# Optimization experiments

Measured on AMD Instinct MI355X. Metric: run time of the kernel, lower is better.

Reference implementation:

```python
import jax, jax.numpy as jnp
import numpy as np

N = 50000          # neuron_count
NNZ = 1_600_000    # edges (avg degree 32)
B = 32             # batch
L = 3              # CONNECTOME_LAYER_NUMBER


def setup_inputs() -> dict:
    key = jax.random.key(0)
    k1, k2, k3, k4, k5 = jax.random.split(key, 5)
    x = jax.random.normal(k1, (B, N), dtype=jnp.float32)
    adj_vals = jax.random.uniform(k2, (NNZ,), dtype=jnp.float32)
    w_vals = jax.random.uniform(k3, (NNZ,), dtype=jnp.float32)
    bias = jnp.ones((N,), dtype=jnp.float32)
    row = jax.random.randint(k4, (NNZ,), 0, N, dtype=jnp.int32)
    col = jax.random.randint(k5, (NNZ,), 0, N, dtype=jnp.int32)
    return {"x": x, "adj_vals": adj_vals, "w_vals": w_vals, "bias": bias,
            "row": row, "col": col}


def _spmm(vals, row, col, dense, n):
    # (sparse NxN) @ dense [N, B] via gather + segment_sum scatter
    contrib = vals[:, None] * dense[col]          # [nnz, B]
    return jax.ops.segment_sum(contrib, row, num_segments=n)


def reference(x, adj_vals, w_vals, bias, row, col):
    # Original per layer: x = ((A @ W) @ x^T)^T + bias.
    # We use associativity: (A @ W) @ x^T == A @ (W @ x^T), avoiding the
    # explicit SpGEMM while computing the same linear map.
    n = bias.shape[0]
    xt = x.T                                      # [N, B]
    for _ in range(L):
        wx = _spmm(w_vals, row, col, xt, n)       # W @ x^T -> [N, B]
        xt = _spmm(adj_vals, row, col, wx, n)     # A @ (W @ x^T)
        xt = xt + bias[:, None]                   # broadcast bias over batch
    return xt.T                                   # [B, N]
```

## Files before the change

kernel.cpp:

```cpp
#include <hip/hip_runtime.h>


#define NN 50000
#define NNZ_E 1600000
#define NB (NN * 32)
#define CHUNK 6144
#define NBLK1 ((NNZ_E + CHUNK - 1) / CHUNK)
#define NBIN ((NN + 127) / 128)
#define NH (NBIN * NBLK1)
#define CAP2 5120
#define BCAP 6144
#define LENP (NBIN * BCAP)
#define LEN2 (LENP / 2)
#define SCAN_NBLK ((NH + 255) / 256)

__device__ __forceinline__ int clampi(int v, int hi) {
    v = v < 0 ? 0 : v;
    return v > hi ? hi : v;
}

__device__ __forceinline__ unsigned short f2h(float v) {
    union { _Float16 h; unsigned short u; } cv;
    cv.h = (_Float16)v;
    return cv.u;
}

__device__ __forceinline__ float kv_val(unsigned kv) {
    union { unsigned short u; _Float16 h; } cv;
    cv.u = (unsigned short)(kv >> 16);
    return (float)cv.h;
}

__global__ __launch_bounds__(256) void hist_kernel(const int* __restrict__ row,
                                                   int* __restrict__ hist1) {
    __shared__ int h[NBIN];
    int blk = blockIdx.x, tid = threadIdx.x;
    for (int j = tid; j < NBIN; j += 256) h[j] = 0;
    __syncthreads();
    int base = blk * CHUNK;
    int n = NNZ_E - base; if (n > CHUNK) n = CHUNK;
    for (int i = tid; i < n; i += 256)
        atomicAdd(&h[clampi(row[base + i], NN - 1) >> 7], 1);
    __syncthreads();
    for (int j = tid; j < NBIN; j += 256) hist1[j * NBLK1 + blk] = h[j];
}

__global__ void scan_local_kernel(int* __restrict__ data, int n, int* __restrict__ bsum) {
    __shared__ int s[256];
    int i = blockIdx.x * 256 + threadIdx.x;
    int v = (i < n) ? data[i] : 0;
    s[threadIdx.x] = v;
    __syncthreads();
    for (int off = 1; off < 256; off <<= 1) {
        int t = (threadIdx.x >= off) ? s[threadIdx.x - off] : 0;
        __syncthreads();
        s[threadIdx.x] += t;
        __syncthreads();
    }
    if (i < n) data[i] = s[threadIdx.x] - v;
    if (threadIdx.x == 255) bsum[blockIdx.x] = s[threadIdx.x];
}

__global__ void scan_tops_kernel(int* __restrict__ bsum, int m) {
    __shared__ int s[512];
    int t = threadIdx.x;
    int v = (t < m) ? bsum[t] : 0;
    s[t] = v;
    __syncthreads();
    for (int off = 1; off < 512; off <<= 1) {
        int u = (t >= off) ? s[t - off] : 0;
        __syncthreads();
        s[t] += u;
        __syncthreads();
    }
    if (t < m) bsum[t] = s[t] - v;
}

__global__ void fin_add_kernel(int* __restrict__ data, int n, const int* __restrict__ bsum) {
    int i = blockIdx.x * blockDim.x + threadIdx.x;
    if (i < n) data[i] += bsum[i >> 8];
}

__global__ void binstart_kernel(const int* __restrict__ hist1, int* __restrict__ binstart) {
    int j = blockIdx.x * blockDim.x + threadIdx.x;
    if (j < NBIN) binstart[j] = hist1[j * NBLK1];
    if (j == 0) binstart[NBIN] = NNZ_E;
}

__global__ __launch_bounds__(256) void pass1_kernel(
        const int* __restrict__ row, const int* __restrict__ col,
        const float* __restrict__ a, const float* __restrict__ w,
        const int* __restrict__ hist1_off,
        unsigned* __restrict__ k1, unsigned* __restrict__ aw1) {
    __shared__ int h[NBIN];
    __shared__ int hscan[NBIN];
    __shared__ int hoff[NBIN];
    __shared__ int s256[256];
    __shared__ unsigned sKey[CHUNK];
    __shared__ unsigned sAW[CHUNK];
    int blk = blockIdx.x, tid = threadIdx.x;
    int base = blk * CHUNK;
    int n = NNZ_E - base; if (n > CHUNK) n = CHUNK;

    for (int j = tid; j < NBIN; j += 256) {
        h[j] = 0;
        hoff[j] = hist1_off[j * NBLK1 + blk];
    }
    __syncthreads();
    for (int i = tid; i < n; i += 256)
        atomicAdd(&h[clampi(row[base + i], NN - 1) >> 7], 1);
    __syncthreads();
    int j0 = tid * 2, j1 = tid * 2 + 1;
    int c0 = (j0 < NBIN) ? h[j0] : 0;
    int c1 = (j1 < NBIN) ? h[j1] : 0;
    int tsum = c0 + c1;
    s256[tid] = tsum;
    __syncthreads();
    for (int off = 1; off < 256; off <<= 1) {
        int t = (tid >= off) ? s256[tid - off] : 0;
        __syncthreads();
        s256[tid] += t;
        __syncthreads();
    }
    int ex = s256[tid] - tsum;
    __syncthreads();
    if (j0 < NBIN) { hscan[j0] = ex;      h[j0] = ex; }
    if (j1 < NBIN) { hscan[j1] = ex + c0; h[j1] = ex + c0; }
    __syncthreads();
    for (int i = tid; i < n; i += 256) {
        int r = clampi(row[base + i], NN - 1);
        int c = clampi(col[base + i], NN - 1);
        int bin = r >> 7;
        int p = atomicAdd(&h[bin], 1);
        p = clampi(p, n - 1);
        sKey[p] = ((unsigned)r << 16) | (unsigned)c;
        sAW[p] = ((unsigned)f2h(a[base + i]) << 16) | (unsigned)f2h(w[base + i]);
    }
    __syncthreads();
    for (int p = tid; p < n; p += 256) {
        unsigned key = sKey[p];
        int bin = (int)(key >> 23);
        int d = clampi(hoff[bin] + (p - hscan[bin]), NNZ_E - 1);
        k1[d] = key;
        aw1[d] = sAW[p];
    }
}

__global__ __launch_bounds__(256) void pass2_kernel(
        const unsigned* __restrict__ k1, const unsigned* __restrict__ aw1,
        const int* __restrict__ binstart,
        unsigned* __restrict__ kvA2, unsigned* __restrict__ kvW2,
        unsigned* __restrict__ row_desc) {
    __shared__ unsigned sKey[CAP2];
    __shared__ unsigned sAW[CAP2];
    __shared__ int rh[128];
    __shared__ int rs[128];
    __shared__ int cur[128];
    int bin = blockIdx.x, tid = threadIdx.x;
    int r0 = bin << 7;
    int rows = NN - r0; if (rows > 128) rows = 128;
    int base = clampi(binstart[bin], NNZ_E);
    int size = clampi(binstart[bin + 1], NNZ_E) - base;
    size = clampi(size, CAP2);
    int pbase = bin * BCAP;

    if (tid < 128) rh[tid] = 0;
    __syncthreads();
    for (int i = tid; i < size; i += 256) {
        unsigned key = k1[base + i];
        atomicAdd(&rh[(key >> 16) & 127], 1);
        sKey[i] = key;
        sAW[i] = aw1[base + i];
    }
    __syncthreads();
    int cnt  = (tid < 128) ? rh[tid] : 0;
    int plen = (cnt + 7) & ~7;
    if (tid < 128) rs[tid] = plen;
    __syncthreads();
    for (int off = 1; off < 128; off <<= 1) {
        int t = (tid >= off && tid < 128) ? rs[tid - off] : 0;
        __syncthreads();
        if (tid < 128) rs[tid] += t;
        __syncthreads();
    }
    int rofs = (tid < 128) ? clampi(rs[tid] - plen, BCAP - 8) : 0;
    if (tid < 128) cur[tid] = rofs;
    if (tid < rows)
        row_desc[r0 + tid] = (unsigned)(pbase + rofs) | ((unsigned)(plen >> 3) << 24);
    __syncthreads();
    for (int i = tid; i < size; i += 256) {
        unsigned key = sKey[i];
        unsigned aw  = sAW[i];
        int rl = (key >> 16) & 127;
        int p = atomicAdd(&cur[rl], 1);
        p = clampi(p, BCAP - 1);
        unsigned c = key & 0xFFFFu;
        kvA2[pbase + p] = (aw & 0xFFFF0000u) | c;
        kvW2[pbase + p] = (aw << 16) | c;
    }
    __syncthreads();
    if (tid < rows) {
        int pl = (rh[tid] + 7) & ~7;
        for (int q = rh[tid]; q < pl; ++q) {
            int d = clampi(rofs + q, BCAP - 1);
            kvA2[pbase + d] = 0u;
            kvW2[pbase + d] = 0u;
        }
    }
}

__global__ void transpose_in_kernel(const float* __restrict__ x,
                                    _Float16* __restrict__ xt) {
    int i = blockIdx.x * blockDim.x + threadIdx.x;
    if (i < NB) {
        int n = i >> 5;
        int b = i & 31;
        xt[i] = (_Float16)x[b * NN + n];
    }
}

template <int WITH_BIAS>
__global__ __launch_bounds__(256) void spmm_kernel(
        const uint2* __restrict__ kv2, const unsigned* __restrict__ row_desc,
        const _Float16* __restrict__ in, _Float16* __restrict__ out,
        const float* __restrict__ bias, float outScale, float biasScale) {
    int t = blockIdx.x * 256 + threadIdx.x;
    int r = t >> 5;
    int b = t & 31;
    if (r >= NN) return;
    unsigned d = row_desc[r];
    int niter = (int)(d >> 24);
    int base2 = clampi((int)(d & 0xFFFFFFu), LENP - 8) >> 1;
    float acc0 = 0.0f;
    float acc1 = 0.0f;
    uint2 k2[4];
    if (niter > 0) {
#pragma unroll
        for (int q = 0; q < 4; ++q) k2[q] = kv2[base2 + q];
    }
    for (int it = 0; it < niter; ++it) {
        unsigned k[8];
#pragma unroll
        for (int q = 0; q < 4; ++q) { k[2 * q] = k2[q].x; k[2 * q + 1] = k2[q].y; }
        float g[8];
#pragma unroll
        for (int j = 0; j < 8; ++j) g[j] = (float)in[((k[j] & 0xFFFFu) << 5) + b];
        if (it + 1 < niter) {
            int nb2 = base2 + (it + 1) * 4;
#pragma unroll
            for (int q = 0; q < 4; ++q) k2[q] = kv2[nb2 + q];
        }
#pragma unroll
        for (int j = 0; j < 8; ++j) {
            if (j & 1) acc1 += kv_val(k[j]) * g[j];
            else       acc0 += kv_val(k[j]) * g[j];
        }
    }
    float res = (acc0 + acc1) * outScale;
    if (WITH_BIAS) res += bias[r] * biasScale;
    out[(r << 5) + b] = (_Float16)res;
}

__global__ void transpose_out_kernel(const _Float16* __restrict__ xt,
                                     float* __restrict__ out) {
    int i = blockIdx.x * blockDim.x + threadIdx.x;
    if (i < NB) {
        int b = i / NN;
        int n = i - b * NN;
        out[i] = (float)xt[(n << 5) + b] * 16777216.0f;
    }
}

extern "C" void kernel_launch(void* const* d_in, const int* in_sizes, int n_in,
                              void* d_out, int out_size, void* d_ws, size_t ws_size,
                              hipStream_t stream) {
    const float* x        = (const float*)d_in[0];
    const float* adj_vals = (const float*)d_in[1];
    const float* w_vals   = (const float*)d_in[2];
    const float* bias     = (const float*)d_in[3];
    const int*   row      = (const int*)d_in[4];
    const int*   col      = (const int*)d_in[5];
    float* out = (float*)d_out;

    unsigned*  k1        = (unsigned*)d_ws;
    unsigned*  aw1       = k1 + NNZ_E;
    unsigned*  kvA2      = aw1 + NNZ_E;
    unsigned*  kvW2      = kvA2 + LENP;
    _Float16*  xt16      = (_Float16*)(kvW2 + LENP);
    _Float16*  tmp16     = xt16 + NB;
    int*   hist1         = (int*)(tmp16 + NB);
    int*   bsumB         = hist1 + NH;
    int*   binstart      = bsumB + 512;
    unsigned* row_desc   = (unsigned*)(binstart + NBIN + 8);

    const int BS = 256;
    const int grid_nb = (NB + BS - 1) / BS;

    hist_kernel<<<NBLK1, BS, 0, stream>>>(row, hist1);
    scan_local_kernel<<<SCAN_NBLK, BS, 0, stream>>>(hist1, NH, bsumB);
    scan_tops_kernel<<<1, 512, 0, stream>>>(bsumB, SCAN_NBLK);
    fin_add_kernel<<<SCAN_NBLK, BS, 0, stream>>>(hist1, NH, bsumB);
    binstart_kernel<<<(NBIN + 1 + BS - 1) / BS, BS, 0, stream>>>(hist1, binstart);

    pass1_kernel<<<NBLK1, BS, 0, stream>>>(row, col, adj_vals, w_vals,
                                           hist1, k1, aw1);
    pass2_kernel<<<NBIN, BS, 0, stream>>>(k1, aw1, binstart, kvA2, kvW2, row_desc);

    const uint2* kvA = (const uint2*)kvA2;
    const uint2* kvW = (const uint2*)kvW2;

    transpose_in_kernel<<<grid_nb, BS, 0, stream>>>(x, xt16);
    const float r256 = 1.0f / 256.0f;
    float biasScale = 1.0f;
    for (int layer = 0; layer < 3; ++layer) {
        biasScale *= r256;
        spmm_kernel<0><<<grid_nb, BS, 0, stream>>>(kvW, row_desc, xt16, tmp16,
                                                   nullptr, 1.0f, 0.0f);
        spmm_kernel<1><<<grid_nb, BS, 0, stream>>>(kvA, row_desc, tmp16, xt16,
                                                   bias, r256, biasScale);
    }
    transpose_out_kernel<<<grid_nb, BS, 0, stream>>>(xt16, out);
}
```

Baseline: 285.4 us.

## Use 8 threads per row with 64-bit gathers and sort rows by length

```diff
diff --git a/kernel.cpp b/kernel.cpp
--- a/kernel.cpp
+++ b/kernel.cpp
@@ -11,7 +11,6 @@
 #define CAP2 5120
 #define BCAP 6144
 #define LENP (NBIN * BCAP)
-#define LEN2 (LENP / 2)
 #define SCAN_NBLK ((NH + 255) / 256)
 
 __device__ __forceinline__ int clampi(int v, int hi) {
@@ -25,10 +24,10 @@
     return cv.u;
 }
 
-__device__ __forceinline__ float kv_val(unsigned kv) {
+__device__ __forceinline__ _Float16 kv_val_h(unsigned kv) {
     union { unsigned short u; _Float16 h; } cv;
     cv.u = (unsigned short)(kv >> 16);
-    return (float)cv.h;
+    return cv.h;
 }
 
 __global__ __launch_bounds__(256) void hist_kernel(const int* __restrict__ row,
@@ -150,12 +149,14 @@
         const unsigned* __restrict__ k1, const unsigned* __restrict__ aw1,
         const int* __restrict__ binstart,
         unsigned* __restrict__ kvA2, unsigned* __restrict__ kvW2,
-        unsigned* __restrict__ row_desc) {
+        unsigned* __restrict__ sdesc, int* __restrict__ srow) {
     __shared__ unsigned sKey[CAP2];
     __shared__ unsigned sAW[CAP2];
     __shared__ int rh[128];
     __shared__ int rs[128];
     __shared__ int cur[128];
+    __shared__ int rofsS[128];
+    __shared__ int cnt64[64];
     int bin = blockIdx.x, tid = threadIdx.x;
     int r0 = bin << 7;
     int rows = NN - r0; if (rows > 128) rows = 128;
@@ -165,6 +166,7 @@
     int pbase = bin * BCAP;
 
     if (tid < 128) rh[tid] = 0;
+    if (tid < 64) cnt64[tid] = 0;
     __syncthreads();
     for (int i = tid; i < size; i += 256) {
         unsigned key = k1[base + i];
@@ -184,9 +186,22 @@
         __syncthreads();
     }
     int rofs = (tid < 128) ? clampi(rs[tid] - plen, BCAP - 8) : 0;
-    if (tid < 128) cur[tid] = rofs;
-    if (tid < rows)
-        row_desc[r0 + tid] = (unsigned)(pbase + rofs) | ((unsigned)(plen >> 3) << 24);
+    if (tid < 128) { cur[tid] = rofs; rofsS[tid] = rofs; }
+    int niter = plen >> 3;
+    int skey = clampi(niter, 63);
+    if (tid < rows) atomicAdd(&cnt64[skey], 1);
+    __syncthreads();
+    if (tid == 0) {
+        int acc = 0;
+        for (int q = 0; q < 64; ++q) { int v = cnt64[q]; cnt64[q] = acc; acc += v; }
+    }
+    __syncthreads();
+    if (tid < rows) {
+        int si = atomicAdd(&cnt64[skey], 1);
+        si = clampi(si, rows - 1);
+        sdesc[r0 + si] = (unsigned)(pbase + rofs) | ((unsigned)niter << 24);
+        srow[r0 + si]  = r0 + tid;
+    }
     __syncthreads();
     for (int i = tid; i < size; i += 256) {
         unsigned key = sKey[i];
@@ -202,7 +217,7 @@
     if (tid < rows) {
         int pl = (rh[tid] + 7) & ~7;
         for (int q = rh[tid]; q < pl; ++q) {
-            int d = clampi(rofs + q, BCAP - 1);
+            int d = clampi(rofsS[tid] + q, BCAP - 1);
             kvA2[pbase + d] = 0u;
             kvW2[pbase + d] = 0u;
         }
@@ -221,18 +236,19 @@
 
 template <int WITH_BIAS>
 __global__ __launch_bounds__(256) void spmm_kernel(
-        const uint2* __restrict__ kv2, const unsigned* __restrict__ row_desc,
-        const _Float16* __restrict__ in, _Float16* __restrict__ out,
+        const uint2* __restrict__ kv2, const unsigned* __restrict__ sdesc,
+        const int* __restrict__ srow,
+        const uint2* __restrict__ in64, uint2* __restrict__ out64,
         const float* __restrict__ bias, float outScale, float biasScale) {
     int t = blockIdx.x * 256 + threadIdx.x;
-    int r = t >> 5;
-    int b = t & 31;
-    if (r >= NN) return;
-    unsigned d = row_desc[r];
+    int g = t >> 3;
+    int l = t & 7;
+    if (g >= NN) return;
+    unsigned d = sdesc[g];
+    int r = clampi(srow[g], NN - 1);
     int niter = (int)(d >> 24);
     int base2 = clampi((int)(d & 0xFFFFFFu), LENP - 8) >> 1;
-    float acc0 = 0.0f;
-    float acc1 = 0.0f;
+    float a0 = 0.0f, a1 = 0.0f, a2 = 0.0f, a3 = 0.0f;
     uint2 k2[4];
     if (niter > 0) {
 #pragma unroll
@@ -242,9 +258,9 @@
         unsigned k[8];
 #pragma unroll
         for (int q = 0; q < 4; ++q) { k[2 * q] = k2[q].x; k[2 * q + 1] = k2[q].y; }
-        float g[8];
-#pragma unroll
-        for (int j = 0; j < 8; ++j) g[j] = (float)in[((k[j] & 0xFFFFu) << 5) + b];
+        uint2 gd[8];
+#pragma unroll
+        for (int j = 0; j < 8; ++j) gd[j] = in64[((k[j] & 0xFFFFu) << 3) + l];
         if (it + 1 < niter) {
             int nb2 = base2 + (it + 1) * 4;
 #pragma unroll
@@ -252,13 +268,25 @@
         }
 #pragma unroll
         for (int j = 0; j < 8; ++j) {
-            if (j & 1) acc1 += kv_val(k[j]) * g[j];
-            else       acc0 += kv_val(k[j]) * g[j];
+            _Float16 vh = kv_val_h(k[j]);
+            union { uint2 u; _Float16 h[4]; } cv;
+            cv.u = gd[j];
+            a0 += (float)vh * (float)cv.h[0];
+            a1 += (float)vh * (float)cv.h[1];
+            a2 += (float)vh * (float)cv.h[2];
+            a3 += (float)vh * (float)cv.h[3];
         }
     }
-    float res = (acc0 + acc1) * outScale;
-    if (WITH_BIAS) res += bias[r] * biasScale;
-    out[(r << 5) + b] = (_Float16)res;
+    float r0 = a0 * outScale, r1 = a1 * outScale;
+    float r2 = a2 * outScale, r3 = a3 * outScale;
+    if (WITH_BIAS) {
+        float bb = bias[r] * biasScale;
+        r0 += bb; r1 += bb; r2 += bb; r3 += bb;
+    }
+    union { uint2 u; _Float16 h[4]; } o;
+    o.h[0] = (_Float16)r0; o.h[1] = (_Float16)r1;
+    o.h[2] = (_Float16)r2; o.h[3] = (_Float16)r3;
+    out64[(r << 3) + l] = o.u;
 }
 
 __global__ void transpose_out_kernel(const _Float16* __restrict__ xt,
@@ -291,10 +319,12 @@
     int*   hist1         = (int*)(tmp16 + NB);
     int*   bsumB         = hist1 + NH;
     int*   binstart      = bsumB + 512;
-    unsigned* row_desc   = (unsigned*)(binstart + NBIN + 8);
+    unsigned* sdesc      = (unsigned*)(binstart + NBIN + 8);
+    int*      srow       = (int*)(sdesc + NN + 8);
 
     const int BS = 256;
-    const int grid_nb = (NB + BS - 1) / BS;
+    const int grid_nb   = (NB + BS - 1) / BS;
+    const int grid_spmm = (NN * 8 + BS - 1) / BS;
 
     hist_kernel<<<NBLK1, BS, 0, stream>>>(row, hist1);
     scan_local_kernel<<<SCAN_NBLK, BS, 0, stream>>>(hist1, NH, bsumB);
@@ -304,20 +334,25 @@
 
     pass1_kernel<<<NBLK1, BS, 0, stream>>>(row, col, adj_vals, w_vals,
                                            hist1, k1, aw1);
-    pass2_kernel<<<NBIN, BS, 0, stream>>>(k1, aw1, binstart, kvA2, kvW2, row_desc);
+    pass2_kernel<<<NBIN, BS, 0, stream>>>(k1, aw1, binstart, kvA2, kvW2,
+                                          sdesc, srow);
 
     const uint2* kvA = (const uint2*)kvA2;
     const uint2* kvW = (const uint2*)kvW2;
+    const uint2* xtg  = (const uint2*)xt16;
+    uint2*       xtgw = (uint2*)xt16;
+    const uint2* tmg  = (const uint2*)tmp16;
+    uint2*       tmgw = (uint2*)tmp16;
 
     transpose_in_kernel<<<grid_nb, BS, 0, stream>>>(x, xt16);
     const float r256 = 1.0f / 256.0f;
     float biasScale = 1.0f;
     for (int layer = 0; layer < 3; ++layer) {
         biasScale *= r256;
-        spmm_kernel<0><<<grid_nb, BS, 0, stream>>>(kvW, row_desc, xt16, tmp16,
-                                                   nullptr, 1.0f, 0.0f);
-        spmm_kernel<1><<<grid_nb, BS, 0, stream>>>(kvA, row_desc, tmp16, xt16,
-                                                   bias, r256, biasScale);
+        spmm_kernel<0><<<grid_spmm, BS, 0, stream>>>(kvW, sdesc, srow, xtg, tmgw,
+                                                     nullptr, 1.0f, 0.0f);
+        spmm_kernel<1><<<grid_spmm, BS, 0, stream>>>(kvA, sdesc, srow, tmg, xtgw,
+                                                     bias, r256, biasScale);
     }
     transpose_out_kernel<<<grid_nb, BS, 0, stream>>>(xt16, out);
 }
```

New measurement: 261.5 us. -8.4%, faster.
